# Kernel tuning notes

Hardware: AMD Instinct MI355X
Metric: run time of the kernel (lower is better)

Reference implementation:

```python
import jax, jax.numpy as jnp
import numpy as np
import math

B, S, E = 16, 600, 300   # batch, seq_len, enc_len
H, NC = 512, 2           # hidden, classes
D = S * E                # archi[0] = 180000


def setup_inputs() -> dict:
    key = jax.random.key(0)
    ks = jax.random.split(key, 7)
    x = jax.random.normal(ks[0], (B, S, E), dtype=jnp.float32)
    y = jax.random.randint(ks[1], (B,), 0, NC)
    # neurons initialized to zeros (init_neurons)
    n0 = jnp.zeros((B, S, E), jnp.float32)
    n1 = jnp.zeros((B, H), jnp.float32)
    n2 = jnp.zeros((B, NC), jnp.float32)
    # Linear weights (torch layout: [out, in]), Kaiming-uniform-like scale 1/sqrt(fan_in)
    W0 = jax.random.uniform(ks[2], (E, E), jnp.float32, -1.0, 1.0) / math.sqrt(E)
    W1 = jax.random.uniform(ks[3], (H, D), jnp.float32, -1.0, 1.0) / math.sqrt(D)
    b1 = jax.random.uniform(ks[4], (H,), jnp.float32, -1.0, 1.0) / math.sqrt(D)
    W2 = jax.random.uniform(ks[5], (NC, H), jnp.float32, -1.0, 1.0) / math.sqrt(H)
    b2 = jax.random.uniform(ks[6], (NC,), jnp.float32, -1.0, 1.0) / math.sqrt(H)
    return dict(x=x, y=y, n0=n0, n1=n1, n2=n2, W0=W0, W1=W1, b1=b1, W2=W2, b2=b2, T=3)


def reference(x, y, n0, n1, n2, W0, W1, b1, W2, b2, T):
    # EqProp free-phase relaxation (beta = 0.0, forward default).
    # Analytic dPhi/dneurons replaces torch.autograd.grad:
    scale = 1.0 / math.sqrt(E)
    Wx = jnp.einsum('bse,fe->bsf', x, W0)  # synapses[0](x), constant across steps
    for _ in range(T):
        g0 = Wx + (n1 @ W1).reshape(B, S, E)              # dPhi/dn0
        g1 = n0.reshape(B, D) @ W1.T + b1 + n2 @ W2       # dPhi/dn1
        g2 = n1 @ W2.T + b2                               # dPhi/dn2 (beta=0)
        # hand-coded attention update for neuron 0: Q=g0, K=V=x
        attn = jax.nn.softmax(scale * jnp.einsum('bse,bte->bst', g0, x), axis=-1)
        n0 = jnp.einsum('bst,bte->bse', attn, x)
        n1 = jnp.tanh(g1)
        n2 = jnp.tanh(g2)
    return n0, n1, n2
```

## Files before the change

### kernel.cpp

```cpp
#include <hip/hip_runtime.h>
#include <math.h>

#define DD 180000L
#define HH 512
#define BB 16
#define SS 600
#define EE 300
#define SP 608
#define EP 320

typedef unsigned short u16;
typedef __attribute__((ext_vector_type(8))) __bf16 bf16x8;
typedef __attribute__((ext_vector_type(4))) float f32x4;

__device__ __forceinline__ u16 f2bf(float f) {
  union { float f; unsigned int u; } x; x.f = f;
  unsigned int r = (x.u + 0x7FFFu + ((x.u >> 16) & 1u)) >> 16;
  return (u16)r;
}

__global__ __launch_bounds__(256) void k_conv_x(const float* __restrict__ x,
                                                u16* __restrict__ xb, u16* __restrict__ xt) {
  __shared__ u16 tl[32][33];
  int b = blockIdx.z;
  int tt = blockIdx.x * 32, ee = blockIdx.y * 32;
  int lx = threadIdx.x & 31, ly = threadIdx.x >> 5;
#pragma unroll
  for (int i = 0; i < 4; ++i) {
    int t = tt + ly + i * 8, e = ee + lx;
    float v = (t < SS && e < EE) ? x[((long)b * SS + t) * EE + e] : 0.f;
    u16 h = f2bf(v);
    xb[((long)b * SP + t) * EP + e] = h;
    tl[ly + i * 8][lx] = h;
  }
  __syncthreads();
#pragma unroll
  for (int i = 0; i < 4; ++i) {
    int e = ee + ly + i * 8, t = tt + lx;
    xt[((long)b * EP + e) * SP + t] = tl[lx][ly + i * 8];
  }
}

__global__ __launch_bounds__(256) void k_conv_w0(const float* __restrict__ W0, u16* __restrict__ w0b) {
  int idx = blockIdx.x * 256 + threadIdx.x;
  int f = idx / EP, e = idx % EP;
  float v = (f < EE && e < EE) ? W0[f * EE + e] : 0.f;
  w0b[idx] = f2bf(v);
}

__global__ __launch_bounds__(256) void k_gemm_nt(
    const u16* __restrict__ A, int lda, long sA, int Arows,
    const u16* __restrict__ B, int ldb, long sB, int Brows,
    float* __restrict__ C, int ldc, long sC, int Mv, int Nv, int K,
    u16* __restrict__ Cb, int ldcb, long sCb) {
  int bz = blockIdx.z;
  int m0 = blockIdx.x * 64, n0 = blockIdx.y * 64;
  int lane = threadIdx.x & 63, wv = threadIdx.x >> 6;
  int wm = m0 + (wv >> 1) * 32, wn = n0 + (wv & 1) * 32;
  int q = lane >> 4, ln = lane & 15;
  const u16* Ab = A + (long)bz * sA;
  const u16* Bb = B + (long)bz * sB;
  long arow0 = (long)min(wm + ln, Arows - 1) * lda;
  long arow1 = (long)min(wm + 16 + ln, Arows - 1) * lda;
  long brow0 = (long)min(wn + ln, Brows - 1) * ldb;
  long brow1 = (long)min(wn + 16 + ln, Brows - 1) * ldb;
  f32x4 acc00 = {0.f,0.f,0.f,0.f}, acc01 = acc00, acc10 = acc00, acc11 = acc00;
  int ksteps = (K + 31) >> 5;
  for (int kk = 0; kk < ksteps; ++kk) {
    int k0 = kk * 32 + q * 8;
    bf16x8 a0 = *(const bf16x8*)(Ab + arow0 + k0);
    bf16x8 a1 = *(const bf16x8*)(Ab + arow1 + k0);
    bf16x8 b0 = *(const bf16x8*)(Bb + brow0 + k0);
    bf16x8 bv1 = *(const bf16x8*)(Bb + brow1 + k0);
    acc00 = __builtin_amdgcn_mfma_f32_16x16x32_bf16(a0, b0,  acc00, 0, 0, 0);
    acc01 = __builtin_amdgcn_mfma_f32_16x16x32_bf16(a0, bv1, acc01, 0, 0, 0);
    acc10 = __builtin_amdgcn_mfma_f32_16x16x32_bf16(a1, b0,  acc10, 0, 0, 0);
    acc11 = __builtin_amdgcn_mfma_f32_16x16x32_bf16(a1, bv1, acc11, 0, 0, 0);
  }
  float* Cp = C + (long)bz * sC;
  u16* Cbp = Cb ? (Cb + (long)bz * sCb) : (u16*)0;
#pragma unroll
  for (int sm = 0; sm < 2; ++sm) {
#pragma unroll
    for (int sn = 0; sn < 2; ++sn) {
      f32x4 acc = (sm == 0) ? ((sn == 0) ? acc00 : acc01) : ((sn == 0) ? acc10 : acc11);
#pragma unroll
      for (int r = 0; r < 4; ++r) {
        int m = wm + sm * 16 + q * 4 + r;
        int n = wn + sn * 16 + ln;
        if (m < Mv && n < Nv) {
          float v = acc[r];
          Cp[(long)m * ldc + n] = v;
          if (Cbp) Cbp[(long)m * ldcb + n] = f2bf(v);
        }
      }
    }
  }
}

#define BN 256
#define BK 64
#define NCH 704

__global__ __launch_bounds__(256) void k_fused_w1(
    const float* __restrict__ W1, const float* __restrict__ n1f,
    const float* __restrict__ n0f, const float* __restrict__ Wx,
    u16* __restrict__ g0b, float* __restrict__ part) {
  __shared__ u16 wt[BK][BN + 8];
  __shared__ u16 n1s[BB][HH + 8];
  __shared__ u16 n0s[BB][BN + 8];
  int tid = threadIdx.x;
  long d0 = (long)blockIdx.x * BN;
#pragma unroll
  for (int i = 0; i < 8; ++i) {
    int f = i * 256 + tid;
    int b = f >> 7, c = (f & 127) * 4;
    float4 v = *(const float4*)(n1f + b * HH + c);
    n1s[b][c] = f2bf(v.x); n1s[b][c + 1] = f2bf(v.y);
    n1s[b][c + 2] = f2bf(v.z); n1s[b][c + 3] = f2bf(v.w);
  }
#pragma unroll
  for (int i = 0; i < 4; ++i) {
    int f = i * 256 + tid;
    int b = f >> 6, c = (f & 63) * 4;
    long d = d0 + c;
    float4 v = {0.f,0.f,0.f,0.f};
    if (d < DD) v = *(const float4*)(n0f + (long)b * DD + d);
    n0s[b][c] = f2bf(v.x); n0s[b][c + 1] = f2bf(v.y);
    n0s[b][c + 2] = f2bf(v.z); n0s[b][c + 3] = f2bf(v.w);
  }
  int lane = tid & 63, wv = tid >> 6, q = lane >> 4, ln = lane & 15;
  f32x4 acc0[4] = {{0.f,0.f,0.f,0.f},{0.f,0.f,0.f,0.f},{0.f,0.f,0.f,0.f},{0.f,0.f,0.f,0.f}};
  for (int s = 0; s < 8; ++s) {
    int h0 = s * BK;
    __syncthreads();
#pragma unroll
    for (int i = 0; i < 16; ++i) {
      int f = i * 256 + tid;
      int r = f >> 6, c = (f & 63) * 4;
      long d = d0 + c;
      float4 v = {0.f,0.f,0.f,0.f};
      if (d < DD) v = *(const float4*)(W1 + (long)(h0 + r) * DD + d);
      wt[r][c] = f2bf(v.x); wt[r][c + 1] = f2bf(v.y);
      wt[r][c + 2] = f2bf(v.z); wt[r][c + 3] = f2bf(v.w);
    }
    __syncthreads();
#pragma unroll
    for (int kst = 0; kst < 2; ++kst) {
      bf16x8 af = *(const bf16x8*)(&n1s[ln][h0 + kst * 32 + q * 8]);
#pragma unroll
      for (int nt = 0; nt < 4; ++nt) {
        int dc = wv * 64 + nt * 16 + ln;
        bf16x8 bv;
#pragma unroll
        for (int j = 0; j < 8; ++j) bv[j] = *(const __bf16*)(&wt[kst * 32 + q * 8 + j][dc]);
        acc0[nt] = __builtin_amdgcn_mfma_f32_16x16x32_bf16(af, bv, acc0[nt], 0, 0, 0);
      }
    }
    f32x4 acc1 = {0.f,0.f,0.f,0.f};
#pragma unroll
    for (int kst = 0; kst < 8; ++kst) {
      bf16x8 af = *(const bf16x8*)(&n0s[ln][kst * 32 + q * 8]);
      bf16x8 bv = *(const bf16x8*)(&wt[wv * 16 + ln][kst * 32 + q * 8]);
      acc1 = __builtin_amdgcn_mfma_f32_16x16x32_bf16(af, bv, acc1, 0, 0, 0);
    }
    long pb = (long)blockIdx.x * 8192;
#pragma unroll
    for (int r = 0; r < 4; ++r) {
      int b = q * 4 + r, h = h0 + wv * 16 + ln;
      part[pb + b * HH + h] = acc1[r];
    }
  }
#pragma unroll
  for (int nt = 0; nt < 4; ++nt) {
#pragma unroll
    for (int r = 0; r < 4; ++r) {
      int b = q * 4 + r;
      long d = d0 + wv * 64 + nt * 16 + ln;
      if (d < DD) {
        float val = Wx[(long)b * DD + d] + acc0[nt][r];
        int sI = (int)(d / EE), e = (int)(d % EE);
        g0b[((long)b * SS + sI) * EP + e] = f2bf(val);
      }
    }
  }
}

#define SWZB(r) ((((r) >> 1) & 7) << 4)

__global__ __launch_bounds__(256, 2) void k_attn(
    const u16* __restrict__ Qg, const u16* __restrict__ Kg,
    const u16* __restrict__ Vtg, float* __restrict__ O, float scale) {
  __shared__ u16 P[16 * SP];
  __shared__ float red[2][4][16];
  int orig = blockIdx.x + blockIdx.y * gridDim.x;
  int wg = (orig & 7) * 76 + (orig >> 3);
  int tile = wg % 38, b = wg / 38;
  int tid = threadIdx.x;
  int w = tid >> 6, lane = tid & 63;
  int q = lane >> 4, ln = lane & 15, q4 = q * 4;
  const u16* Qb = Qg + (long)b * SS * EP;
  const u16* Kb = Kg + (long)b * SP * EP;
  const u16* Vb = Vtg + (long)b * EP * SP;

  int qrow = min(tile * 16 + ln, SS - 1);
  bf16x8 qf[10];
#pragma unroll
  for (int kk = 0; kk < 10; ++kk)
    qf[kk] = *(const bf16x8*)(Qb + (long)qrow * EP + kk * 32 + q * 8);

  f32x4 s[10];
#pragma unroll
  for (int i = 0; i < 10; ++i) {
    int j = w + 4 * i;
    f32x4 sa = {0.f, 0.f, 0.f, 0.f}, sb = {0.f, 0.f, 0.f, 0.f};
    if (j < 38) {
      const u16* Kr = Kb + (long)(j * 16 + ln) * EP + q * 8;
#pragma unroll
      for (int kk = 0; kk < 10; kk += 2) {
        bf16x8 k0 = *(const bf16x8*)(Kr + kk * 32);
        bf16x8 k1 = *(const bf16x8*)(Kr + kk * 32 + 32);
        sa = __builtin_amdgcn_mfma_f32_16x16x32_bf16(qf[kk], k0, sa, 0, 0, 0);
        sb = __builtin_amdgcn_mfma_f32_16x16x32_bf16(qf[kk + 1], k1, sb, 0, 0, 0);
      }
    }
    s[i] = sa + sb;
  }

  float mx[4] = {-3e38f, -3e38f, -3e38f, -3e38f};
#pragma unroll
  for (int i = 0; i < 10; ++i) {
    int j = w + 4 * i;
    if (j < 38) {
      bool msk = (j == 37) && (ln >= 8);
#pragma unroll
      for (int r = 0; r < 4; ++r) mx[r] = fmaxf(mx[r], msk ? -3e38f : s[i][r]);
    }
  }
#pragma unroll
  for (int off = 8; off; off >>= 1)
#pragma unroll
    for (int r = 0; r < 4; ++r) mx[r] = fmaxf(mx[r], __shfl_xor(mx[r], off));
  if (ln == 0) {
#pragma unroll
    for (int r = 0; r < 4; ++r) red[0][w][q4 + r] = mx[r];
  }
  __syncthreads();
#pragma unroll
  for (int r = 0; r < 4; ++r)
    mx[r] = fmaxf(fmaxf(red[0][0][q4 + r], red[0][1][q4 + r]),
                  fmaxf(red[0][2][q4 + r], red[0][3][q4 + r]));
  float sm[4] = {0.f, 0.f, 0.f, 0.f};
#pragma unroll
  for (int i = 0; i < 10; ++i) {
    int j = w + 4 * i;
    if (j < 38) {
      bool msk = (j == 37) && (ln >= 8);
#pragma unroll
      for (int r = 0; r < 4; ++r) {
        float e = msk ? 0.f : __expf(scale * (s[i][r] - mx[r]));
        s[i][r] = e;
        sm[r] += e;
      }
    }
  }
#pragma unroll
  for (int off = 8; off; off >>= 1)
#pragma unroll
    for (int r = 0; r < 4; ++r) sm[r] += __shfl_xor(sm[r], off);
  if (ln == 0) {
#pragma unroll
    for (int r = 0; r < 4; ++r) red[1][w][q4 + r] = sm[r];
  }
  __syncthreads();
#pragma unroll
  for (int r = 0; r < 4; ++r)
    sm[r] = 1.f / (red[1][0][q4 + r] + red[1][1][q4 + r] +
                   red[1][2][q4 + r] + red[1][3][q4 + r]);

#pragma unroll
  for (int i = 0; i < 10; ++i) {
    int j = w + 4 * i;
    if (j < 38) {
#pragma unroll
      for (int r = 0; r < 4; ++r) {
        int row = q4 + r, t = j * 16 + ln;
        unsigned byt = (unsigned)row * 1216 + (unsigned)t * 2;
        P[(byt ^ SWZB(row)) >> 1] = f2bf(s[i][r] * sm[r]);
      }
    }
  }
  __syncthreads();

  f32x4 acc[5];
#pragma unroll
  for (int i = 0; i < 5; ++i) acc[i] = (f32x4){0.f, 0.f, 0.f, 0.f};
#pragma unroll
  for (int kt = 0; kt < 19; ++kt) {
    unsigned byt = (unsigned)ln * 1216 + (unsigned)kt * 64 + (unsigned)q * 16;
    bf16x8 pa = *(const bf16x8*)(&P[(byt ^ SWZB(ln)) >> 1]);
#pragma unroll
    for (int i = 0; i < 5; ++i) {
      int nt = w + 4 * i;
      if (nt < 19) {
        bf16x8 bv = *(const bf16x8*)(Vb + (long)(nt * 16 + ln) * SP + kt * 32 + q * 8);
        acc[i] = __builtin_amdgcn_mfma_f32_16x16x32_bf16(pa, bv, acc[i], 0, 0, 0);
      }
    }
  }

  float* Ob = O + (long)b * SS * EE;
  int m0 = tile * 16 + q4;
#pragma unroll
  for (int i = 0; i < 5; ++i) {
    int nt = w + 4 * i;
    if (nt < 19) {
#pragma unroll
      for (int r = 0; r < 4; ++r) {
        int m = m0 + r, n = nt * 16 + ln;
        if (m < SS && n < EE) Ob[(long)m * EE + n] = acc[i][r];
      }
    }
  }
}

__global__ __launch_bounds__(256) void k_init(const float* __restrict__ b1, const float* __restrict__ b2,
                                              float* __restrict__ n1, float* __restrict__ n2) {
  int idx = blockIdx.x * 256 + threadIdx.x;
  n1[idx] = tanhf(b1[idx & 511]);
  if (idx < 32) n2[idx] = tanhf(b2[idx & 1]);
}

__global__ __launch_bounds__(64) void k_g2(const float* __restrict__ n1old, const float* __restrict__ W2,
                                           const float* __restrict__ b2, float* __restrict__ n2out) {
  int b = blockIdx.x >> 1, c = blockIdx.x & 1, lane = threadIdx.x;
  float s = 0.f;
#pragma unroll
  for (int i = 0; i < 8; ++i) { int h = lane + i * 64; s += n1old[b * HH + h] * W2[c * HH + h]; }
  for (int off = 32; off; off >>= 1) s += __shfl_down(s, off);
  if (lane == 0) n2out[b * 2 + c] = tanhf(s + b2[c]);
}

__global__ __launch_bounds__(256) void k_reduce1(const float* __restrict__ part, float* __restrict__ part2) {
  int idx = blockIdx.x * 256 + threadIdx.x;
  int sl = blockIdx.y;
  float s = 0.f;
  int c0 = sl * 88;
#pragma unroll 4
  for (int c = 0; c < 88; ++c) s += part[(long)(c0 + c) * 8192 + idx];
  part2[(long)sl * 8192 + idx] = s;
}

__global__ __launch_bounds__(256) void k_reduce2(const float* __restrict__ part2, const float* __restrict__ b1,
                                                 const float* __restrict__ W2, const float* __restrict__ n2old,
                                                 float* __restrict__ n1out) {
  int idx = blockIdx.x * 256 + threadIdx.x;
  int b = idx >> 9, h = idx & 511;
  float s = b1[h] + n2old[b * 2] * W2[h] + n2old[b * 2 + 1] * W2[HH + h];
#pragma unroll
  for (int sl = 0; sl < 8; ++sl) s += part2[(long)sl * 8192 + idx];
  n1out[idx] = tanhf(s);
}

extern "C" void kernel_launch(void* const* d_in, const int* in_sizes, int n_in,
                              void* d_out, int out_size, void* d_ws, size_t ws_size,
                              hipStream_t stream) {
  const float* x  = (const float*)d_in[0];
  const float* W0 = (const float*)d_in[5];
  const float* W1 = (const float*)d_in[6];
  const float* b1 = (const float*)d_in[7];
  const float* W2 = (const float*)d_in[8];
  const float* b2 = (const float*)d_in[9];

  float* out_n0 = (float*)d_out;
  float* out_n1 = out_n0 + 16L * SS * EE;
  float* out_n2 = out_n1 + 16L * HH;

  char* w = (char*)d_ws;
  auto take = [&](size_t bytes) { char* p = w; w += (bytes + 255) & ~(size_t)255; return p; };
  u16*   xb    = (u16*)take(16L * SP * EP * 2);
  u16*   xt    = (u16*)take(16L * EP * SP * 2);
  u16*   w0b   = (u16*)take((size_t)EP * EP * 2);
  float* Wx    = (float*)take(16L * SS * EE * 4);
  u16*   g0b   = (u16*)take(16L * SS * EP * 2);
  float* part  = (float*)take((size_t)NCH * 8192 * 4);
  float* part2 = (float*)take(8L * 8192 * 4);
  float* n1A   = (float*)take(8192 * 4);
  float* n1B   = (float*)take(8192 * 4);
  float* n2A   = (float*)take(256);
  float* n2B   = (float*)take(256);

  const float scale = 1.0f / sqrtf((float)EE);

  k_conv_x<<<dim3(19, 10, 16), 256, 0, stream>>>(x, xb, xt);
  k_conv_w0<<<400, 256, 0, stream>>>(W0, w0b);
  k_gemm_nt<<<dim3(10, 5, 16), 256, 0, stream>>>(xb, EP, (long)SP * EP, SP,
                                                 w0b, EP, 0, EP,
                                                 Wx, EE, (long)SS * EE, SS, EE, EE,
                                                 g0b, EP, (long)SS * EP);
  k_init<<<32, 256, 0, stream>>>(b1, b2, n1A, n2A);

  for (int it = 0; it < 3; ++it) {
    if (it > 0) {
      const float* n1old = (it == 1) ? n1A : n1B;
      const float* n2old = (it == 1) ? n2A : n2B;
      float* n2new = (it == 1) ? n2B : out_n2;
      float* n1new = (it == 1) ? n1B : out_n1;
      k_g2<<<32, 64, 0, stream>>>(n1old, W2, b2, n2new);
      k_fused_w1<<<NCH, 256, 0, stream>>>(W1, n1old, out_n0, Wx, g0b, part);
      k_reduce1<<<dim3(32, 8), 256, 0, stream>>>(part, part2);
      k_reduce2<<<32, 256, 0, stream>>>(part2, b1, W2, n2old, n1new);
    }
    k_attn<<<dim3(38, 16), 256, 0, stream>>>(g0b, xb, xt, out_n0, scale);
  }
}
```

Baseline: 959.6 us.

## Cache bf16 W1 copy across iterations, prefetch tiles, swizzle LDS

Result: faster. 884.0 us (-7.9%).

```diff
diff --git a/kernel.cpp b/kernel.cpp
--- a/kernel.cpp
+++ b/kernel.cpp
@@ -8,6 +8,7 @@
 #define EE 300
 #define SP 608
 #define EP 320
+#define WPD 180224L
 
 typedef unsigned short u16;
 typedef __attribute__((ext_vector_type(8))) __bf16 bf16x8;
@@ -101,9 +102,12 @@
 #define BN 256
 #define BK 64
 #define NCH 704
-
-__global__ __launch_bounds__(256) void k_fused_w1(
-    const float* __restrict__ W1, const float* __restrict__ n1f,
+#define SWZW(r) ((unsigned)(((((r) & 7) ^ (((r) >> 3) & 7))) << 4))
+
+template <int SRC>
+__global__ __launch_bounds__(256, 2) void k_fw1(
+    const float* __restrict__ W1, const u16* __restrict__ w1b_in,
+    u16* __restrict__ w1b_out, const float* __restrict__ n1f,
     const float* __restrict__ n0f, const float* __restrict__ Wx,
     u16* __restrict__ g0b, float* __restrict__ part) {
   __shared__ u16 wt[BK][BN + 8];
@@ -111,6 +115,7 @@
   __shared__ u16 n0s[BB][BN + 8];
   int tid = threadIdx.x;
   long d0 = (long)blockIdx.x * BN;
+  char* wtb = (char*)&wt[0][0];
 #pragma unroll
   for (int i = 0; i < 8; ++i) {
     int f = i * 256 + tid;
@@ -130,19 +135,64 @@
     n0s[b][c + 2] = f2bf(v.z); n0s[b][c + 3] = f2bf(v.w);
   }
   int lane = tid & 63, wv = tid >> 6, q = lane >> 4, ln = lane & 15;
+
+  float4 pfA[16];
+  bf16x8 pfB[8];
+  if constexpr (SRC == 0) {
+#pragma unroll
+    for (int i = 0; i < 16; ++i) {
+      int f = i * 256 + tid; int r = f >> 6, c = (f & 63) * 4;
+      long d = d0 + c;
+      float4 v = {0.f,0.f,0.f,0.f};
+      if (d < DD) v = *(const float4*)(W1 + (long)r * DD + d);
+      pfA[i] = v;
+    }
+  } else {
+#pragma unroll
+    for (int i = 0; i < 8; ++i) {
+      int f = i * 256 + tid; int r = f >> 5, c = (f & 31) * 8;
+      pfB[i] = *(const bf16x8*)(w1b_in + (long)r * WPD + d0 + c);
+    }
+  }
+
   f32x4 acc0[4] = {{0.f,0.f,0.f,0.f},{0.f,0.f,0.f,0.f},{0.f,0.f,0.f,0.f},{0.f,0.f,0.f,0.f}};
   for (int s = 0; s < 8; ++s) {
     int h0 = s * BK;
     __syncthreads();
-#pragma unroll
-    for (int i = 0; i < 16; ++i) {
-      int f = i * 256 + tid;
-      int r = f >> 6, c = (f & 63) * 4;
-      long d = d0 + c;
-      float4 v = {0.f,0.f,0.f,0.f};
-      if (d < DD) v = *(const float4*)(W1 + (long)(h0 + r) * DD + d);
-      wt[r][c] = f2bf(v.x); wt[r][c + 1] = f2bf(v.y);
-      wt[r][c + 2] = f2bf(v.z); wt[r][c + 3] = f2bf(v.w);
+    if constexpr (SRC == 0) {
+#pragma unroll
+      for (int i = 0; i < 16; ++i) {
+        int f = i * 256 + tid; int r = f >> 6, c = (f & 63) * 4;
+        ushort4 h;
+        h.x = f2bf(pfA[i].x); h.y = f2bf(pfA[i].y);
+        h.z = f2bf(pfA[i].z); h.w = f2bf(pfA[i].w);
+        *(ushort4*)(wtb + (unsigned)r * 528 + (((unsigned)(c * 2)) ^ SWZW(r))) = h;
+        *(ushort4*)(w1b_out + (long)(h0 + r) * WPD + d0 + c) = h;
+      }
+    } else {
+#pragma unroll
+      for (int i = 0; i < 8; ++i) {
+        int f = i * 256 + tid; int r = f >> 5, c = (f & 31) * 8;
+        *(bf16x8*)(wtb + (unsigned)r * 528 + (((unsigned)(c * 2)) ^ SWZW(r))) = pfB[i];
+      }
+    }
+    if (s < 7) {
+      if constexpr (SRC == 0) {
+#pragma unroll
+        for (int i = 0; i < 16; ++i) {
+          int f = i * 256 + tid; int r = f >> 6, c = (f & 63) * 4;
+          long d = d0 + c;
+          float4 v = {0.f,0.f,0.f,0.f};
+          if (d < DD) v = *(const float4*)(W1 + (long)(h0 + BK + r) * DD + d);
+          pfA[i] = v;
+        }
+      } else {
+#pragma unroll
+        for (int i = 0; i < 8; ++i) {
+          int f = i * 256 + tid; int r = f >> 5, c = (f & 31) * 8;
+          pfB[i] = *(const bf16x8*)(w1b_in + (long)(h0 + BK + r) * WPD + d0 + c);
+        }
+      }
     }
     __syncthreads();
 #pragma unroll
@@ -153,16 +203,24 @@
         int dc = wv * 64 + nt * 16 + ln;
         bf16x8 bv;
 #pragma unroll
-        for (int j = 0; j < 8; ++j) bv[j] = *(const __bf16*)(&wt[kst * 32 + q * 8 + j][dc]);
+        for (int j = 0; j < 8; ++j) {
+          int rr = kst * 32 + q * 8 + j;
+          bv[j] = *(const __bf16*)(wtb + (unsigned)rr * 528 + (((unsigned)(dc * 2)) ^ SWZW(rr)));
+        }
         acc0[nt] = __builtin_amdgcn_mfma_f32_16x16x32_bf16(af, bv, acc0[nt], 0, 0, 0);
       }
     }
     f32x4 acc1 = {0.f,0.f,0.f,0.f};
-#pragma unroll
-    for (int kst = 0; kst < 8; ++kst) {
-      bf16x8 af = *(const bf16x8*)(&n0s[ln][kst * 32 + q * 8]);
-      bf16x8 bv = *(const bf16x8*)(&wt[wv * 16 + ln][kst * 32 + q * 8]);
-      acc1 = __builtin_amdgcn_mfma_f32_16x16x32_bf16(af, bv, acc1, 0, 0, 0);
+    {
+      int row = wv * 16 + ln;
+      unsigned sw = SWZW(row);
+#pragma unroll
+      for (int kst = 0; kst < 8; ++kst) {
+        bf16x8 af = *(const bf16x8*)(&n0s[ln][kst * 32 + q * 8]);
+        bf16x8 bvv = *(const bf16x8*)(wtb + (unsigned)row * 528 +
+                                      (((unsigned)((kst * 32 + q * 8) * 2)) ^ sw));
+        acc1 = __builtin_amdgcn_mfma_f32_16x16x32_bf16(af, bvv, acc1, 0, 0, 0);
+      }
     }
     long pb = (long)blockIdx.x * 8192;
 #pragma unroll
@@ -383,6 +441,7 @@
   u16*   w0b   = (u16*)take((size_t)EP * EP * 2);
   float* Wx    = (float*)take(16L * SS * EE * 4);
   u16*   g0b   = (u16*)take(16L * SS * EP * 2);
+  u16*   w1b   = (u16*)take((size_t)HH * WPD * 2);
   float* part  = (float*)take((size_t)NCH * 8192 * 4);
   float* part2 = (float*)take(8L * 8192 * 4);
   float* n1A   = (float*)take(8192 * 4);
@@ -407,7 +466,10 @@
       float* n2new = (it == 1) ? n2B : out_n2;
       float* n1new = (it == 1) ? n1B : out_n1;
       k_g2<<<32, 64, 0, stream>>>(n1old, W2, b2, n2new);
-      k_fused_w1<<<NCH, 256, 0, stream>>>(W1, n1old, out_n0, Wx, g0b, part);
+      if (it == 1)
+        k_fw1<0><<<NCH, 256, 0, stream>>>(W1, (const u16*)0, w1b, n1old, out_n0, Wx, g0b, part);
+      else
+        k_fw1<1><<<NCH, 256, 0, stream>>>(W1, w1b, (u16*)0, n1old, out_n0, Wx, g0b, part);
       k_reduce1<<<dim3(32, 8), 256, 0, stream>>>(part, part2);
       k_reduce2<<<32, 256, 0, stream>>>(part2, b1, W2, n2old, n1new);
     }
```
